# Kernel tuning notes

Measured on AMD Instinct MI355X. Metric: run time of the kernel, lower is better.

Reference implementation:

```python
import jax, jax.numpy as jnp
import numpy as np

N_NODES = 100000
N_EDGES = 3200000
F_IN = 256
H1 = 128   # growth_rate * bn_size
H2 = 32    # growth_rate
BN_EPS = 1e-5


def _gin_bn_relu(x, edge_index, Wa, ba, Wb, bb, gamma, beta):
    # GINConv (eps=0): h_i = MLP(x_i + sum_{j in N(i)} x_j)
    src, dst = edge_index[0], edge_index[1]
    agg = jax.ops.segment_sum(x[src], dst, num_segments=x.shape[0])  # [N, F]
    h = x + agg
    # nn1: Linear -> ReLU -> Linear
    h = jnp.maximum(h @ Wa + ba, 0.0)
    h = h @ Wb + bb
    # BatchNorm1d (training-mode batch stats over nodes)
    mean = h.mean(axis=0)
    var = h.var(axis=0)  # biased, matches torch BN normalization
    h = (h - mean) * jax.lax.rsqrt(var + BN_EPS) * gamma + beta
    return jnp.maximum(h, 0.0)


def setup_inputs() -> dict:
    key = jax.random.key(0)
    ks = jax.random.split(key, 12)
    x = jax.random.normal(ks[0], (N_NODES, F_IN), dtype=jnp.float32)
    edge_index = jax.random.randint(ks[1], (2, N_EDGES), 0, N_NODES, dtype=jnp.int64)

    def lin(k, fin, fout):
        s = 1.0 / np.sqrt(fin)
        return jax.random.uniform(k, (fin, fout), jnp.float32, -s, s)

    return {
        "x": x,
        "edge_index": edge_index,
        "W1a": lin(ks[2], F_IN, H1), "b1a": jnp.zeros((H1,), jnp.float32),
        "W1b": lin(ks[3], H1, H1),   "b1b": jnp.zeros((H1,), jnp.float32),
        "g1": jnp.ones((H1,), jnp.float32), "be1": jnp.zeros((H1,), jnp.float32),
        "W2a": lin(ks[4], H1, H2),   "b2a": jnp.zeros((H2,), jnp.float32),
        "W2b": lin(ks[5], H2, H2),   "b2b": jnp.zeros((H2,), jnp.float32),
        "g2": jnp.ones((H2,), jnp.float32), "be2": jnp.zeros((H2,), jnp.float32),
    }


def reference(x, edge_index, W1a, b1a, W1b, b1b, g1, be1,
              W2a, b2a, W2b, b2b, g2, be2):
    # data.x is a single tensor -> [x]; torch.cat([x], 1) == x (concat is a no-op)
    h = _gin_bn_relu(x, edge_index, W1a, b1a, W1b, b1b, g1, be1)   # [N, 128]
    h = _gin_bn_relu(h, edge_index, W2a, b2a, W2b, b2b, g2, be2)   # [N, 32]
    return h
```

## Files before the change

### kernel.cpp

```cpp
#include <hip/hip_runtime.h>

#define F_IN 256
#define H1 128
#define H2 32
#define BN_EPS 1e-5f
#define BSHIFT 8
#define BCAP 16384
#define CHUNK 4096
#define NSHARD 8

typedef short bf16x8 __attribute__((ext_vector_type(8)));
typedef float f32x4 __attribute__((ext_vector_type(4)));

__device__ __forceinline__ ushort f2bf(float f) {
    uint u = __float_as_uint(f);
    return (ushort)((u + 0x7FFFu + ((u >> 16) & 1u)) >> 16);
}
__device__ __forceinline__ float bf2f(ushort h) {
    return __uint_as_float((uint)h << 16);
}
__device__ __forceinline__ uint pack2(float a, float b) {
    return (uint)f2bf(a) | ((uint)f2bf(b) << 16);
}
__device__ __forceinline__ void unpack2(uint u, float& a, float& b) {
    a = __uint_as_float(u << 16);
    b = __uint_as_float(u & 0xFFFF0000u);
}
__device__ __forceinline__ int clampN(int v, int N) {
    return v < 0 ? 0 : (v >= N ? N - 1 : v);
}

__global__ __launch_bounds__(256) void super0_k(
    const float* __restrict__ W1a, const float* __restrict__ W1b,
    const float* __restrict__ W2a, const float* __restrict__ W2b,
    ushort* __restrict__ w1aT, ushort* __restrict__ w1bT,
    ushort* __restrict__ w2aT, ushort* __restrict__ w2bT,
    int* __restrict__ bucket_cursor, float* __restrict__ sums1,
    float* __restrict__ sums2) {
    const int tid = threadIdx.x;
    if (blockIdx.x == 212) {
        for (int i = tid; i < 512; i += 256) bucket_cursor[i] = 0;
        for (int i = tid; i < NSHARD * 2 * H1; i += 256) sums1[i] = 0.f;
        for (int i = tid; i < NSHARD * 2 * H2; i += 256) sums2[i] = 0.f;
        return;
    }
    int idx = blockIdx.x * 256 + tid;
    if (idx < 32768) {
        int k = idx >> 7, c = idx & 127;
        w1aT[c * 256 + k] = f2bf(W1a[idx]);
    } else if (idx < 49152) {
        int t = idx - 32768;
        int k = t >> 7, c = t & 127;
        w1bT[c * 128 + k] = f2bf(W1b[t]);
    } else if (idx < 53248) {
        int t = idx - 49152;
        int k = t >> 5, c = t & 31;
        w2aT[c * 128 + k] = f2bf(W2a[t]);
    } else if (idx < 54272) {
        int t = idx - 53248;
        int k = t >> 5, c = t & 31;
        w2bT[c * 32 + k] = f2bf(W2b[t]);
    }
}

__global__ __launch_bounds__(256) void binA_k(const int* __restrict__ eb,
                                              int E, int N, int NBUCK,
                                              int* __restrict__ bucket_cursor,
                                              uint* __restrict__ rec) {
    __shared__ int lcnt[512];
    __shared__ int lbase[512];
    __shared__ uint lrec[CHUNK];
    __shared__ ushort lbk[CHUNK];
    __shared__ ushort lrk[CHUNK];
    __shared__ int nzf;
    const int tid = threadIdx.x;
    const int cbase = blockIdx.x * CHUNK;
    const int cnum = min(CHUNK, E - cbase);
    if (cnum <= 0) return;
    if (tid == 0) nzf = 0;
    __syncthreads();
    {
        int i = tid * (CHUNK / 256);
        if (i < cnum && eb[2 * (cbase + i) + 1] != 0) atomicAdd(&nzf, 1);
    }
    for (int i = tid; i < NBUCK; i += 256) lcnt[i] = 0;
    __syncthreads();
    const int is64 = (nzf == 0);
    for (int i = tid; i < cnum; i += 256) {
        int e = cbase + i;
        int s = is64 ? eb[2 * e] : eb[e];
        int d = is64 ? eb[2 * (E + e)] : eb[E + e];
        s = clampN(s, N);
        d = clampN(d, N);
        int bk = d >> BSHIFT;
        int rk = atomicAdd(&lcnt[bk], 1);
        lrec[i] = (uint)s | ((uint)(d & 255) << 17);
        lbk[i] = (ushort)bk;
        lrk[i] = (ushort)rk;
    }
    __syncthreads();
    for (int i = tid; i < NBUCK; i += 256)
        if (lcnt[i]) lbase[i] = atomicAdd(&bucket_cursor[i], lcnt[i]);
    __syncthreads();
    for (int i = tid; i < cnum; i += 256) {
        int bk = lbk[i];
        int pos = lbase[bk] + lrk[i];
        if (pos < BCAP) rec[(size_t)bk * BCAP + pos] = lrec[i];
    }
}

__global__ __launch_bounds__(256) void gemm1_k(const float* __restrict__ Af,
                                               const ushort* __restrict__ WT,
                                               ushort* __restrict__ outb, int N) {
    constexpr int K = F_IN, NC = H1, NF = NC / 16;
    const int lane = threadIdx.x & 63;
    const int wave = threadIdx.x >> 6;
    const int row0 = blockIdx.x * 64 + wave * 16;
    const int col = lane & 15;
    const int k0 = (lane >> 4) * 8;
    int arow = row0 + col;
    if (arow >= N) arow = N - 1;

    f32x4 acc[NF];
#pragma unroll
    for (int f = 0; f < NF; ++f) acc[f] = (f32x4){0.f, 0.f, 0.f, 0.f};
#pragma unroll
    for (int kc = 0; kc < K; kc += 32) {
        const float* ap = &Af[(size_t)arow * K + kc + k0];
        float4 p = *(const float4*)ap;
        float4 q = *(const float4*)(ap + 4);
        bf16x8 af;
        af[0] = (short)f2bf(p.x); af[1] = (short)f2bf(p.y);
        af[2] = (short)f2bf(p.z); af[3] = (short)f2bf(p.w);
        af[4] = (short)f2bf(q.x); af[5] = (short)f2bf(q.y);
        af[6] = (short)f2bf(q.z); af[7] = (short)f2bf(q.w);
#pragma unroll
        for (int f = 0; f < NF; ++f) {
            bf16x8 bf = *(const bf16x8*)&WT[(size_t)(f * 16 + col) * K + kc + k0];
            acc[f] = __builtin_amdgcn_mfma_f32_16x16x32_bf16(af, bf, acc[f], 0, 0, 0);
        }
    }
    const int crow = row0 + (lane >> 4) * 4;
#pragma unroll
    for (int f = 0; f < NF; ++f) {
        const int c = f * 16 + col;
#pragma unroll
        for (int j = 0; j < 4; ++j) {
            int rr = crow + j;
            if (rr < N) outb[(size_t)rr * NC + c] = f2bf(acc[f][j]);
        }
    }
}

__global__ __launch_bounds__(256) void binB_k(const uint* __restrict__ rec,
                                              const int* __restrict__ bucket_cursor,
                                              int N, int NBUCK,
                                              int* __restrict__ row_start,
                                              int* __restrict__ esrc) {
    __shared__ int cntA[256];
    __shared__ int cntB[256];
    __shared__ int red[256];
    const int bk = blockIdx.x;
    const int tid = threadIdx.x;
    int part = 0;
    for (int i = tid; i < bk; i += 256) {
        int c = bucket_cursor[i];
        part += (c < BCAP) ? c : BCAP;
    }
    red[tid] = part;
    __syncthreads();
    for (int s = 128; s > 0; s >>= 1) {
        if (tid < s) red[tid] += red[tid + s];
        __syncthreads();
    }
    const int base = red[0];
    int cnt = bucket_cursor[bk];
    if (cnt > BCAP) cnt = BCAP;
    if (bk == NBUCK - 1 && tid == 0) row_start[N] = base + cnt;

    const uint* r = rec + (size_t)bk * BCAP;
    cntA[tid] = 0;
    __syncthreads();
    for (int i = tid; i < cnt; i += 256) atomicAdd(&cntA[r[i] >> 17], 1);
    __syncthreads();
    int* src = cntA;
    int* dst = cntB;
    for (int off = 1; off < 256; off <<= 1) {
        int v = src[tid] + (tid >= off ? src[tid - off] : 0);
        __syncthreads();
        dst[tid] = v;
        __syncthreads();
        int* t = src; src = dst; dst = t;
    }
    const int n0 = bk << BSHIFT;
    {
        int node = n0 + tid;
        if (node < N) row_start[node] = base + (tid ? src[tid - 1] : 0);
    }
    dst[tid] = 0;
    __syncthreads();
    for (int i = tid; i < cnt; i += 256) {
        uint rv = r[i];
        int dl = rv >> 17;
        int rank = atomicAdd(&dst[dl], 1);
        esrc[base + (dl ? src[dl - 1] : 0) + rank] = (int)(rv & 0x1FFFFu);
    }
}

template <int NC, bool BIAS, bool OUT_BF16, bool STATS, int NF>
__device__ __forceinline__ void gemm_epilogue(f32x4* acc, const float* bias,
                                              void* outv, int N, int row0,
                                              int lane, float* sums) {
    __shared__ float ssum[NC];
    __shared__ float ssq[NC];
    if (STATS) {
        if (threadIdx.x < NC) { ssum[threadIdx.x] = 0.f; ssq[threadIdx.x] = 0.f; }
        __syncthreads();
    }
    const int col0 = lane & 15;
    const int crow = row0 + (lane >> 4) * 4;
#pragma unroll
    for (int f = 0; f < NF; ++f) {
        const int c = f * 16 + col0;
        float bv = BIAS ? bias[c] : 0.f;
        float sv = 0.f, qv = 0.f;
#pragma unroll
        for (int j = 0; j < 4; ++j) {
            int rr = crow + j;
            if (rr < N) {
                float v = acc[f][j] + bv;
                if (OUT_BF16) ((ushort*)outv)[(size_t)rr * NC + c] = f2bf(v);
                else          ((float*)outv)[(size_t)rr * NC + c] = v;
                if (STATS) { sv += v; qv += v * v; }
            }
        }
        if (STATS) {
            sv += __shfl_xor(sv, 16); sv += __shfl_xor(sv, 32);
            qv += __shfl_xor(qv, 16); qv += __shfl_xor(qv, 32);
            if ((lane >> 4) == 0) {
                atomicAdd(&ssum[c], sv);
                atomicAdd(&ssq[c], qv);
            }
        }
    }
    if (STATS) {
        __syncthreads();
        if (threadIdx.x < NC) {
            float* sh = sums + (blockIdx.x & (NSHARD - 1)) * 2 * NC;
            atomicAdd(&sh[threadIdx.x], ssum[threadIdx.x]);
            atomicAdd(&sh[NC + threadIdx.x], ssq[threadIdx.x]);
        }
    }
}

template <int K, int NC, bool BIAS, bool OUT_BF16, bool STATS>
__global__ __launch_bounds__(256) void gemm_mfma_k(const ushort* __restrict__ A,
                                                   const ushort* __restrict__ WT,
                                                   const float* __restrict__ bias,
                                                   void* __restrict__ outv, int N,
                                                   float* __restrict__ sums) {
    constexpr int NF = NC / 16;
    const int lane = threadIdx.x & 63;
    const int wave = threadIdx.x >> 6;
    const int row0 = blockIdx.x * 64 + wave * 16;
    const int col = lane & 15;
    const int k0 = (lane >> 4) * 8;
    int arow = row0 + col;
    if (arow >= N) arow = N - 1;

    f32x4 acc[NF];
#pragma unroll
    for (int f = 0; f < NF; ++f) acc[f] = (f32x4){0.f, 0.f, 0.f, 0.f};
#pragma unroll
    for (int kc = 0; kc < K; kc += 32) {
        bf16x8 af = *(const bf16x8*)&A[(size_t)arow * K + kc + k0];
#pragma unroll
        for (int f = 0; f < NF; ++f) {
            bf16x8 bf = *(const bf16x8*)&WT[(size_t)(f * 16 + col) * K + kc + k0];
            acc[f] = __builtin_amdgcn_mfma_f32_16x16x32_bf16(af, bf, acc[f], 0, 0, 0);
        }
    }
    gemm_epilogue<NC, BIAS, OUT_BF16, STATS, NF>(acc, bias, outv, N, row0, lane, sums);
}

template <int K, int NC, bool OUT_BF16>
__global__ __launch_bounds__(256) void gemm_mfma_bnA_k(const ushort* __restrict__ U,
                                                       const ushort* __restrict__ WT,
                                                       const float* __restrict__ sums,
                                                       const float* __restrict__ g,
                                                       const float* __restrict__ be,
                                                       int Nbn,
                                                       void* __restrict__ outv, int N) {
    constexpr int NF = NC / 16;
    __shared__ __align__(16) float lsc[K];
    __shared__ __align__(16) float lsh[K];
    const int tid = threadIdx.x;
    if (tid < K) {
        float s = 0.f, q = 0.f;
#pragma unroll
        for (int sh = 0; sh < NSHARD; ++sh) {
            s += sums[sh * 2 * K + tid];
            q += sums[sh * 2 * K + K + tid];
        }
        float inv_n = 1.f / (float)Nbn;
        float mean = s * inv_n;
        float var = q * inv_n - mean * mean;
        float sc = g[tid] * rsqrtf(var + BN_EPS);
        lsc[tid] = sc;
        lsh[tid] = be[tid] - mean * sc;
    }
    __syncthreads();

    const int lane = tid & 63;
    const int wave = tid >> 6;
    const int row0 = blockIdx.x * 64 + wave * 16;
    const int col = lane & 15;
    const int k0 = (lane >> 4) * 8;
    int arow = row0 + col;
    if (arow >= N) arow = N - 1;

    f32x4 acc[NF];
#pragma unroll
    for (int f = 0; f < NF; ++f) acc[f] = (f32x4){0.f, 0.f, 0.f, 0.f};
#pragma unroll
    for (int kc = 0; kc < K; kc += 32) {
        bf16x8 raw = *(const bf16x8*)&U[(size_t)arow * K + kc + k0];
        float4 c0 = *(const float4*)&lsc[kc + k0];
        float4 c1 = *(const float4*)&lsc[kc + k0 + 4];
        float4 h0 = *(const float4*)&lsh[kc + k0];
        float4 h1 = *(const float4*)&lsh[kc + k0 + 4];
        bf16x8 af;
        af[0] = (short)f2bf(fmaxf(bf2f((ushort)raw[0]) * c0.x + h0.x, 0.f));
        af[1] = (short)f2bf(fmaxf(bf2f((ushort)raw[1]) * c0.y + h0.y, 0.f));
        af[2] = (short)f2bf(fmaxf(bf2f((ushort)raw[2]) * c0.z + h0.z, 0.f));
        af[3] = (short)f2bf(fmaxf(bf2f((ushort)raw[3]) * c0.w + h0.w, 0.f));
        af[4] = (short)f2bf(fmaxf(bf2f((ushort)raw[4]) * c1.x + h1.x, 0.f));
        af[5] = (short)f2bf(fmaxf(bf2f((ushort)raw[5]) * c1.y + h1.y, 0.f));
        af[6] = (short)f2bf(fmaxf(bf2f((ushort)raw[6]) * c1.z + h1.z, 0.f));
        af[7] = (short)f2bf(fmaxf(bf2f((ushort)raw[7]) * c1.w + h1.w, 0.f));
#pragma unroll
        for (int f = 0; f < NF; ++f) {
            bf16x8 bf = *(const bf16x8*)&WT[(size_t)(f * 16 + col) * K + kc + k0];
            acc[f] = __builtin_amdgcn_mfma_f32_16x16x32_bf16(af, bf, acc[f], 0, 0, 0);
        }
    }
    gemm_epilogue<NC, false, OUT_BF16, false, NF>(acc, nullptr, outv, N, row0, lane, nullptr);
}

__global__ void agg_f128b_k(const ushort* __restrict__ T, const int* __restrict__ row_start,
                            const int* __restrict__ esrc, const float* __restrict__ bias,
                            ushort* __restrict__ out, int N) {
    const int hw = (blockIdx.x << 3) | (threadIdx.x >> 5);
    const int lane = threadIdx.x & 31;
    if (hw >= N) return;
    const uint2* T2 = (const uint2*)T;
    uint2 sv = T2[(size_t)hw * 32 + lane];
    float a0, a1, a2, a3;
    unpack2(sv.x, a0, a1);
    unpack2(sv.y, a2, a3);
    int p = row_start[hw];
    const int pe = row_start[hw + 1];
    for (; p + 7 < pe; p += 8) {
        int s0 = esrc[p],     s1 = esrc[p + 1], s2 = esrc[p + 2], s3 = esrc[p + 3];
        int s4 = esrc[p + 4], s5 = esrc[p + 5], s6 = esrc[p + 6], s7 = esrc[p + 7];
        uint2 v0 = T2[(size_t)s0 * 32 + lane];
        uint2 v1 = T2[(size_t)s1 * 32 + lane];
        uint2 v2 = T2[(size_t)s2 * 32 + lane];
        uint2 v3 = T2[(size_t)s3 * 32 + lane];
        uint2 v4 = T2[(size_t)s4 * 32 + lane];
        uint2 v5 = T2[(size_t)s5 * 32 + lane];
        uint2 v6 = T2[(size_t)s6 * 32 + lane];
        uint2 v7 = T2[(size_t)s7 * 32 + lane];
        float x0, x1, x2, x3;
        unpack2(v0.x, x0, x1); unpack2(v0.y, x2, x3);
        a0 += x0; a1 += x1; a2 += x2; a3 += x3;
        unpack2(v1.x, x0, x1); unpack2(v1.y, x2, x3);
        a0 += x0; a1 += x1; a2 += x2; a3 += x3;
        unpack2(v2.x, x0, x1); unpack2(v2.y, x2, x3);
        a0 += x0; a1 += x1; a2 += x2; a3 += x3;
        unpack2(v3.x, x0, x1); unpack2(v3.y, x2, x3);
        a0 += x0; a1 += x1; a2 += x2; a3 += x3;
        unpack2(v4.x, x0, x1); unpack2(v4.y, x2, x3);
        a0 += x0; a1 += x1; a2 += x2; a3 += x3;
        unpack2(v5.x, x0, x1); unpack2(v5.y, x2, x3);
        a0 += x0; a1 += x1; a2 += x2; a3 += x3;
        unpack2(v6.x, x0, x1); unpack2(v6.y, x2, x3);
        a0 += x0; a1 += x1; a2 += x2; a3 += x3;
        unpack2(v7.x, x0, x1); unpack2(v7.y, x2, x3);
        a0 += x0; a1 += x1; a2 += x2; a3 += x3;
    }
    for (; p < pe; ++p) {
        uint2 v = T2[(size_t)esrc[p] * 32 + lane];
        float x0, x1, x2, x3;
        unpack2(v.x, x0, x1); unpack2(v.y, x2, x3);
        a0 += x0; a1 += x1; a2 += x2; a3 += x3;
    }
    const float4 b = ((const float4*)bias)[lane];
    a0 = fmaxf(a0 + b.x, 0.f);
    a1 = fmaxf(a1 + b.y, 0.f);
    a2 = fmaxf(a2 + b.z, 0.f);
    a3 = fmaxf(a3 + b.w, 0.f);
    ((uint2*)out)[(size_t)hw * 32 + lane] = make_uint2(pack2(a0, a1), pack2(a2, a3));
}

__global__ void agg_f32b_k(const ushort* __restrict__ T, const int* __restrict__ row_start,
                           const int* __restrict__ esrc, const float* __restrict__ bias,
                           ushort* __restrict__ out, int N) {
    const int wid = (blockIdx.x << 2) | (threadIdx.x >> 6);
    const int lane = threadIdx.x & 63;
    const int g = lane >> 3, l8 = lane & 7;
    if (wid >= N) return;
    const uint2* T2 = (const uint2*)T;
    float a0 = 0.f, a1 = 0.f, a2 = 0.f, a3 = 0.f;
    const int p0 = row_start[wid];
    const int pe = row_start[wid + 1];
    for (int p = p0 + g; p < pe; p += 8) {
        uint2 v = T2[(size_t)esrc[p] * 8 + l8];
        float x0, x1, x2, x3;
        unpack2(v.x, x0, x1); unpack2(v.y, x2, x3);
        a0 += x0; a1 += x1; a2 += x2; a3 += x3;
    }
#pragma unroll
    for (int off = 8; off < 64; off <<= 1) {
        a0 += __shfl_xor(a0, off);
        a1 += __shfl_xor(a1, off);
        a2 += __shfl_xor(a2, off);
        a3 += __shfl_xor(a3, off);
    }
    if (g == 0) {
        uint2 sv = T2[(size_t)wid * 8 + l8];
        float s0, s1, s2, s3;
        unpack2(sv.x, s0, s1); unpack2(sv.y, s2, s3);
        const float4 b = ((const float4*)bias)[l8];
        a0 = fmaxf(a0 + s0 + b.x, 0.f);
        a1 = fmaxf(a1 + s1 + b.y, 0.f);
        a2 = fmaxf(a2 + s2 + b.z, 0.f);
        a3 = fmaxf(a3 + s3 + b.w, 0.f);
        ((uint2*)out)[(size_t)wid * 8 + l8] = make_uint2(pack2(a0, a1), pack2(a2, a3));
    }
}

template <int F>
__global__ void bnapply_fin_k(const float* __restrict__ U, const float* __restrict__ sums,
                              const float* __restrict__ g, const float* __restrict__ be,
                              int Nbn, float* __restrict__ out, int total4) {
    __shared__ __align__(16) float lsc[F];
    __shared__ __align__(16) float lsh[F];
    const int tid = threadIdx.x;
    if (tid < F) {
        float s = 0.f, q = 0.f;
#pragma unroll
        for (int sh = 0; sh < NSHARD; ++sh) {
            s += sums[sh * 2 * F + tid];
            q += sums[sh * 2 * F + F + tid];
        }
        float inv_n = 1.f / (float)Nbn;
        float mean = s * inv_n;
        float var = q * inv_n - mean * mean;
        float sc = g[tid] * rsqrtf(var + BN_EPS);
        lsc[tid] = sc;
        lsh[tid] = be[tid] - mean * sc;
    }
    __syncthreads();
    const float4* U4 = (const float4*)U;
    float4* O4 = (float4*)out;
    const int stride = gridDim.x * blockDim.x;
    for (int i = blockIdx.x * blockDim.x + tid; i < total4; i += stride) {
        int c4 = (i % (F / 4)) * 4;
        float4 u = U4[i];
        float4 sc = *(const float4*)&lsc[c4];
        float4 sh = *(const float4*)&lsh[c4];
        float4 o;
        o.x = fmaxf(u.x * sc.x + sh.x, 0.f);
        o.y = fmaxf(u.y * sc.y + sh.y, 0.f);
        o.z = fmaxf(u.z * sc.z + sh.z, 0.f);
        o.w = fmaxf(u.w * sc.w + sh.w, 0.f);
        O4[i] = o;
    }
}

extern "C" void kernel_launch(void* const* d_in, const int* in_sizes, int n_in,
                              void* d_out, int out_size, void* d_ws, size_t ws_size,
                              hipStream_t stream) {
    const float* x   = (const float*)d_in[0];
    const int*   eb  = (const int*)d_in[1];
    const float* W1a = (const float*)d_in[2];
    const float* b1a = (const float*)d_in[3];
    const float* W1b = (const float*)d_in[4];
    const float* b1b = (const float*)d_in[5];
    const float* g1  = (const float*)d_in[6];
    const float* be1 = (const float*)d_in[7];
    const float* W2a = (const float*)d_in[8];
    const float* b2a = (const float*)d_in[9];
    const float* W2b = (const float*)d_in[10];
    const float* b2b = (const float*)d_in[11];
    const float* g2  = (const float*)d_in[12];
    const float* be2 = (const float*)d_in[13];
    float* out = (float*)d_out;

    const int N = in_sizes[0] / F_IN;
    const int E = in_sizes[1] / 2;
    const int NBUCK = (N + 255) >> BSHIFT;

    char* w = (char*)d_ws;
    size_t off = 0;
    auto alloc = [&](size_t bytes) -> void* {
        void* p = w + off;
        off = (off + bytes + 255) & ~(size_t)255;
        return p;
    };
    ushort* B0 = (ushort*)alloc((size_t)N * H1 * 2);
    ushort* B1 = (ushort*)alloc((size_t)N * H1 * 2);
    char*   B2 = (char*)alloc((size_t)N * H1 * 4);
    ushort* u1b = (ushort*)B2;
    float*  u2  = (float*)B2;

    int* row_start = (int*)alloc((size_t)(N + 1) * 4);
    int* esrc      = (int*)alloc((size_t)E * 4);
    uint* rec      = (uint*)alloc((size_t)NBUCK * BCAP * 4);
    int* bucket_cursor = (int*)alloc(512 * 4);
    ushort* w1aT = (ushort*)alloc(F_IN * H1 * 2);
    ushort* w1bT = (ushort*)alloc(H1 * H1 * 2);
    ushort* w2aT = (ushort*)alloc(H1 * H2 * 2);
    ushort* w2bT = (ushort*)alloc(H2 * H2 * 2);
    float* sums1 = (float*)alloc(NSHARD * 2 * H1 * 4);
    float* sums2 = (float*)alloc(NSHARD * 2 * H2 * 4);

    const int GB = (E + CHUNK - 1) / CHUNK;
    const int G1 = (N + 63) / 64;

    super0_k<<<213, 256, 0, stream>>>(W1a, W1b, W2a, W2b, w1aT, w1bT, w2aT, w2bT,
                                      bucket_cursor, sums1, sums2);
    binA_k<<<GB, 256, 0, stream>>>(eb, E, N, NBUCK, bucket_cursor, rec);
    gemm1_k<<<G1, 256, 0, stream>>>(x, w1aT, B1, N);
    binB_k<<<NBUCK, 256, 0, stream>>>(rec, bucket_cursor, N, NBUCK, row_start, esrc);
    agg_f128b_k<<<(N + 7) / 8, 256, 0, stream>>>(B1, row_start, esrc, b1a, B0, N);
    gemm_mfma_k<H1, H1, true, true, true><<<G1, 256, 0, stream>>>(B0, w1bT, b1b, u1b, N, sums1);
    gemm_mfma_bnA_k<H1, H2, true><<<G1, 256, 0, stream>>>(u1b, w2aT, sums1, g1, be1, N, B1, N);
    agg_f32b_k<<<(N + 3) / 4, 256, 0, stream>>>(B1, row_start, esrc, b2a, B0, N);
    gemm_mfma_k<H2, H2, true, false, true><<<G1, 256, 0, stream>>>(B0, w2bT, b2b, u2, N, sums2);
    bnapply_fin_k<H2><<<3125, 256, 0, stream>>>(u2, sums2, g2, be2, N, out, N * H2 / 4);
}
```

Before: 387.8 us.

## Merge binB and gemm1 into one launch; rework binA as two-pass count/scatter

binA now counts bucket sizes in a first pass, reserves global ranges, then re-reads the edges and scatters records directly, so the per-chunk shared-memory record staging goes away and the chunk size doubles. binB and the first GEMM become one kernel that assigns blocks by index range, removing a launch and letting the two independent jobs overlap. In exchange, binA reads the destination indices twice, and the write order inside a bucket now depends on atomic order. That is harmless because binB re-sorts within each bucket.

```diff
diff --git a/kernel.cpp b/kernel.cpp
--- a/kernel.cpp
+++ b/kernel.cpp
@@ -6,7 +6,7 @@
 #define BN_EPS 1e-5f
 #define BSHIFT 8
 #define BCAP 16384
-#define CHUNK 4096
+#define CHUNK 8192
 #define NSHARD 8
 
 typedef short bf16x8 __attribute__((ext_vector_type(8)));
@@ -69,9 +69,6 @@
                                               uint* __restrict__ rec) {
     __shared__ int lcnt[512];
     __shared__ int lbase[512];
-    __shared__ uint lrec[CHUNK];
-    __shared__ ushort lbk[CHUNK];
-    __shared__ ushort lrk[CHUNK];
     __shared__ int nzf;
     const int tid = threadIdx.x;
     const int cbase = blockIdx.x * CHUNK;
@@ -86,6 +83,19 @@
     for (int i = tid; i < NBUCK; i += 256) lcnt[i] = 0;
     __syncthreads();
     const int is64 = (nzf == 0);
+    for (int i = tid; i < cnum; i += 256) {
+        int e = cbase + i;
+        int d = is64 ? eb[2 * (E + e)] : eb[E + e];
+        d = clampN(d, N);
+        atomicAdd(&lcnt[d >> BSHIFT], 1);
+    }
+    __syncthreads();
+    for (int i = tid; i < NBUCK; i += 256) {
+        int c = lcnt[i];
+        lbase[i] = c ? atomicAdd(&bucket_cursor[i], c) : 0;
+        lcnt[i] = 0;
+    }
+    __syncthreads();
     for (int i = tid; i < cnum; i += 256) {
         int e = cbase + i;
         int s = is64 ? eb[2 * e] : eb[e];
@@ -93,29 +103,73 @@
         s = clampN(s, N);
         d = clampN(d, N);
         int bk = d >> BSHIFT;
-        int rk = atomicAdd(&lcnt[bk], 1);
-        lrec[i] = (uint)s | ((uint)(d & 255) << 17);
-        lbk[i] = (ushort)bk;
-        lrk[i] = (ushort)rk;
-    }
-    __syncthreads();
-    for (int i = tid; i < NBUCK; i += 256)
-        if (lcnt[i]) lbase[i] = atomicAdd(&bucket_cursor[i], lcnt[i]);
-    __syncthreads();
-    for (int i = tid; i < cnum; i += 256) {
-        int bk = lbk[i];
-        int pos = lbase[bk] + lrk[i];
-        if (pos < BCAP) rec[(size_t)bk * BCAP + pos] = lrec[i];
-    }
-}
-
-__global__ __launch_bounds__(256) void gemm1_k(const float* __restrict__ Af,
-                                               const ushort* __restrict__ WT,
-                                               ushort* __restrict__ outb, int N) {
+        int pos = lbase[bk] + atomicAdd(&lcnt[bk], 1);
+        if (pos < BCAP)
+            rec[(size_t)bk * BCAP + pos] = (uint)s | ((uint)(d & 255) << 17);
+    }
+}
+
+__device__ __forceinline__ void binB_body(int bk, const uint* __restrict__ rec,
+                                          const int* __restrict__ bucket_cursor,
+                                          int N, int NBUCK,
+                                          int* __restrict__ row_start,
+                                          int* __restrict__ esrc) {
+    __shared__ int cntA[256];
+    __shared__ int cntB[256];
+    __shared__ int red[256];
+    const int tid = threadIdx.x;
+    int part = 0;
+    for (int i = tid; i < bk; i += 256) {
+        int c = bucket_cursor[i];
+        part += (c < BCAP) ? c : BCAP;
+    }
+    red[tid] = part;
+    __syncthreads();
+    for (int s = 128; s > 0; s >>= 1) {
+        if (tid < s) red[tid] += red[tid + s];
+        __syncthreads();
+    }
+    const int base = red[0];
+    int cnt = bucket_cursor[bk];
+    if (cnt > BCAP) cnt = BCAP;
+    if (bk == NBUCK - 1 && tid == 0) row_start[N] = base + cnt;
+
+    const uint* r = rec + (size_t)bk * BCAP;
+    cntA[tid] = 0;
+    __syncthreads();
+    for (int i = tid; i < cnt; i += 256) atomicAdd(&cntA[r[i] >> 17], 1);
+    __syncthreads();
+    int* src = cntA;
+    int* dst = cntB;
+    for (int off = 1; off < 256; off <<= 1) {
+        int v = src[tid] + (tid >= off ? src[tid - off] : 0);
+        __syncthreads();
+        dst[tid] = v;
+        __syncthreads();
+        int* t = src; src = dst; dst = t;
+    }
+    const int n0 = bk << BSHIFT;
+    {
+        int node = n0 + tid;
+        if (node < N) row_start[node] = base + (tid ? src[tid - 1] : 0);
+    }
+    dst[tid] = 0;
+    __syncthreads();
+    for (int i = tid; i < cnt; i += 256) {
+        uint rv = r[i];
+        int dl = rv >> 17;
+        int rank = atomicAdd(&dst[dl], 1);
+        esrc[base + (dl ? src[dl - 1] : 0) + rank] = (int)(rv & 0x1FFFFu);
+    }
+}
+
+__device__ __forceinline__ void gemm1_body(int bid, const float* __restrict__ Af,
+                                           const ushort* __restrict__ WT,
+                                           ushort* __restrict__ outb, int N) {
     constexpr int K = F_IN, NC = H1, NF = NC / 16;
     const int lane = threadIdx.x & 63;
     const int wave = threadIdx.x >> 6;
-    const int row0 = blockIdx.x * 64 + wave * 16;
+    const int row0 = bid * 64 + wave * 16;
     const int col = lane & 15;
     const int k0 = (lane >> 4) * 8;
     int arow = row0 + col;
@@ -152,59 +206,15 @@
     }
 }
 
-__global__ __launch_bounds__(256) void binB_k(const uint* __restrict__ rec,
-                                              const int* __restrict__ bucket_cursor,
-                                              int N, int NBUCK,
-                                              int* __restrict__ row_start,
-                                              int* __restrict__ esrc) {
-    __shared__ int cntA[256];
-    __shared__ int cntB[256];
-    __shared__ int red[256];
-    const int bk = blockIdx.x;
-    const int tid = threadIdx.x;
-    int part = 0;
-    for (int i = tid; i < bk; i += 256) {
-        int c = bucket_cursor[i];
-        part += (c < BCAP) ? c : BCAP;
-    }
-    red[tid] = part;
-    __syncthreads();
-    for (int s = 128; s > 0; s >>= 1) {
-        if (tid < s) red[tid] += red[tid + s];
-        __syncthreads();
-    }
-    const int base = red[0];
-    int cnt = bucket_cursor[bk];
-    if (cnt > BCAP) cnt = BCAP;
-    if (bk == NBUCK - 1 && tid == 0) row_start[N] = base + cnt;
-
-    const uint* r = rec + (size_t)bk * BCAP;
-    cntA[tid] = 0;
-    __syncthreads();
-    for (int i = tid; i < cnt; i += 256) atomicAdd(&cntA[r[i] >> 17], 1);
-    __syncthreads();
-    int* src = cntA;
-    int* dst = cntB;
-    for (int off = 1; off < 256; off <<= 1) {
-        int v = src[tid] + (tid >= off ? src[tid - off] : 0);
-        __syncthreads();
-        dst[tid] = v;
-        __syncthreads();
-        int* t = src; src = dst; dst = t;
-    }
-    const int n0 = bk << BSHIFT;
-    {
-        int node = n0 + tid;
-        if (node < N) row_start[node] = base + (tid ? src[tid - 1] : 0);
-    }
-    dst[tid] = 0;
-    __syncthreads();
-    for (int i = tid; i < cnt; i += 256) {
-        uint rv = r[i];
-        int dl = rv >> 17;
-        int rank = atomicAdd(&dst[dl], 1);
-        esrc[base + (dl ? src[dl - 1] : 0) + rank] = (int)(rv & 0x1FFFFu);
-    }
+__global__ __launch_bounds__(256) void super2_k(
+    const uint* __restrict__ rec, const int* __restrict__ bucket_cursor,
+    int N, int NBUCK, int* __restrict__ row_start, int* __restrict__ esrc,
+    const float* __restrict__ x, const ushort* __restrict__ w1aT,
+    ushort* __restrict__ t1b) {
+    if ((int)blockIdx.x < NBUCK)
+        binB_body(blockIdx.x, rec, bucket_cursor, N, NBUCK, row_start, esrc);
+    else
+        gemm1_body(blockIdx.x - NBUCK, x, w1aT, t1b, N);
 }
 
 template <int NC, bool BIAS, bool OUT_BF16, bool STATS, int NF>
@@ -532,8 +542,8 @@
     super0_k<<<213, 256, 0, stream>>>(W1a, W1b, W2a, W2b, w1aT, w1bT, w2aT, w2bT,
                                       bucket_cursor, sums1, sums2);
     binA_k<<<GB, 256, 0, stream>>>(eb, E, N, NBUCK, bucket_cursor, rec);
-    gemm1_k<<<G1, 256, 0, stream>>>(x, w1aT, B1, N);
-    binB_k<<<NBUCK, 256, 0, stream>>>(rec, bucket_cursor, N, NBUCK, row_start, esrc);
+    super2_k<<<NBUCK + G1, 256, 0, stream>>>(rec, bucket_cursor, N, NBUCK,
+                                             row_start, esrc, x, w1aT, B1);
     agg_f128b_k<<<(N + 7) / 8, 256, 0, stream>>>(B1, row_start, esrc, b1a, B0, N);
     gemm_mfma_k<H1, H1, true, true, true><<<G1, 256, 0, stream>>>(B0, w1bT, b1b, u1b, N, sums1);
     gemm_mfma_bnA_k<H1, H2, true><<<G1, 256, 0, stream>>>(u1b, w2aT, sums1, g1, be1, N, B1, N);
```

Measured after the change: 395.5 us. No clear change (+2.0%).

## Fuse CSR bucket finalize with first GEMM and sub-sort edges by source octant

Applied to the files above, without the earlier changes.

Merges the bucket-finalize (binB) and first dense GEMM into one launch, splitting blocks by index so CSR construction and the x@W1a MFMA GEMM run concurrently and one launch gap disappears. binB now sorts each destination's edges into 8 sub-bins by source-index high bits, so neighbour gathers within a row touch nearby source rows. The row-start array grows to 8 entries per node and the aggregation kernels read the stride-8 layout. The cost is larger LDS use in the fused kernel, which can lower occupancy for the GEMM blocks, and a bigger row-start buffer.

```diff
diff --git a/kernel.cpp b/kernel.cpp
--- a/kernel.cpp
+++ b/kernel.cpp
@@ -109,13 +109,80 @@
     }
 }
 
-__global__ __launch_bounds__(256) void gemm1_k(const float* __restrict__ Af,
-                                               const ushort* __restrict__ WT,
-                                               ushort* __restrict__ outb, int N) {
+__device__ __forceinline__ void binB_body(int bk, const uint* __restrict__ rec,
+                                          const int* __restrict__ bucket_cursor,
+                                          int N, int NBUCK,
+                                          int* __restrict__ rs2,
+                                          int* __restrict__ esrc) {
+    __shared__ int cnt[2048];
+    __shared__ int rnk[2048];
+    __shared__ int red[256];
+    const int tid = threadIdx.x;
+    int part = 0;
+    for (int i = tid; i < bk; i += 256) {
+        int c = bucket_cursor[i];
+        part += (c < BCAP) ? c : BCAP;
+    }
+    red[tid] = part;
+    __syncthreads();
+    for (int s = 128; s > 0; s >>= 1) {
+        if (tid < s) red[tid] += red[tid + s];
+        __syncthreads();
+    }
+    const int base = red[0];
+    __syncthreads();
+    int cntb = bucket_cursor[bk];
+    if (cntb > BCAP) cntb = BCAP;
+    if (bk == NBUCK - 1 && tid == 0) rs2[(size_t)N * 8] = base + cntb;
+
+    const uint* r = rec + (size_t)bk * BCAP;
+    for (int i = tid; i < 2048; i += 256) { cnt[i] = 0; rnk[i] = 0; }
+    __syncthreads();
+    for (int i = tid; i < cntb; i += 256) {
+        uint rv = r[i];
+        atomicAdd(&cnt[((rv >> 17) << 3) | ((rv >> 14) & 7u)], 1);
+    }
+    __syncthreads();
+    int loc[8];
+    int s = 0;
+#pragma unroll
+    for (int j = 0; j < 8; ++j) { loc[j] = s; s += cnt[tid * 8 + j]; }
+    const int tot = s;
+    red[tid] = tot;
+    __syncthreads();
+    for (int off = 1; off < 256; off <<= 1) {
+        int t = (tid >= off) ? red[tid - off] : 0;
+        __syncthreads();
+        red[tid] += t;
+        __syncthreads();
+    }
+    const int excl_t = red[tid] - tot;
+    __syncthreads();
+    const int n0 = bk << BSHIFT;
+#pragma unroll
+    for (int j = 0; j < 8; ++j) {
+        int b = tid * 8 + j;
+        int ex = excl_t + loc[j];
+        cnt[b] = ex;
+        int node = n0 + (b >> 3);
+        if (node < N) rs2[(size_t)node * 8 + (b & 7)] = base + ex;
+    }
+    __syncthreads();
+    for (int i = tid; i < cntb; i += 256) {
+        uint rv = r[i];
+        int b = ((rv >> 17) << 3) | ((rv >> 14) & 7u);
+        int pos = cnt[b] + atomicAdd(&rnk[b], 1);
+        esrc[base + pos] = (int)(rv & 0x1FFFFu);
+    }
+}
+
+__device__ __forceinline__ void gemm1_body(int bid, const float* __restrict__ Af,
+                                           const ushort* __restrict__ WT,
+                                           ushort* __restrict__ outb, int N) {
     constexpr int K = F_IN, NC = H1, NF = NC / 16;
     const int lane = threadIdx.x & 63;
     const int wave = threadIdx.x >> 6;
-    const int row0 = blockIdx.x * 64 + wave * 16;
+    const int row0 = bid * 64 + wave * 16;
     const int col = lane & 15;
     const int k0 = (lane >> 4) * 8;
     int arow = row0 + col;
@@ -152,59 +219,15 @@
     }
 }
 
-__global__ __launch_bounds__(256) void binB_k(const uint* __restrict__ rec,
-                                              const int* __restrict__ bucket_cursor,
-                                              int N, int NBUCK,
-                                              int* __restrict__ row_start,
-                                              int* __restrict__ esrc) {
-    __shared__ int cntA[256];
-    __shared__ int cntB[256];
-    __shared__ int red[256];
-    const int bk = blockIdx.x;
-    const int tid = threadIdx.x;
-    int part = 0;
-    for (int i = tid; i < bk; i += 256) {
-        int c = bucket_cursor[i];
-        part += (c < BCAP) ? c : BCAP;
-    }
-    red[tid] = part;
-    __syncthreads();
-    for (int s = 128; s > 0; s >>= 1) {
-        if (tid < s) red[tid] += red[tid + s];
-        __syncthreads();
-    }
-    const int base = red[0];
-    int cnt = bucket_cursor[bk];
-    if (cnt > BCAP) cnt = BCAP;
-    if (bk == NBUCK - 1 && tid == 0) row_start[N] = base + cnt;
-
-    const uint* r = rec + (size_t)bk * BCAP;
-    cntA[tid] = 0;
-    __syncthreads();
-    for (int i = tid; i < cnt; i += 256) atomicAdd(&cntA[r[i] >> 17], 1);
-    __syncthreads();
-    int* src = cntA;
-    int* dst = cntB;
-    for (int off = 1; off < 256; off <<= 1) {
-        int v = src[tid] + (tid >= off ? src[tid - off] : 0);
-        __syncthreads();
-        dst[tid] = v;
-        __syncthreads();
-        int* t = src; src = dst; dst = t;
-    }
-    const int n0 = bk << BSHIFT;
-    {
-        int node = n0 + tid;
-        if (node < N) row_start[node] = base + (tid ? src[tid - 1] : 0);
-    }
-    dst[tid] = 0;
-    __syncthreads();
-    for (int i = tid; i < cnt; i += 256) {
-        uint rv = r[i];
-        int dl = rv >> 17;
-        int rank = atomicAdd(&dst[dl], 1);
-        esrc[base + (dl ? src[dl - 1] : 0) + rank] = (int)(rv & 0x1FFFFu);
-    }
+__global__ __launch_bounds__(256) void super2_k(
+    const uint* __restrict__ rec, const int* __restrict__ bucket_cursor,
+    int N, int NBUCK, int* __restrict__ rs2, int* __restrict__ esrc,
+    const float* __restrict__ x, const ushort* __restrict__ w1aT,
+    ushort* __restrict__ t1b) {
+    if ((int)blockIdx.x < NBUCK)
+        binB_body(blockIdx.x, rec, bucket_cursor, N, NBUCK, rs2, esrc);
+    else
+        gemm1_body(blockIdx.x - NBUCK, x, w1aT, t1b, N);
 }
 
 template <int NC, bool BIAS, bool OUT_BF16, bool STATS, int NF>
@@ -347,7 +370,7 @@
     gemm_epilogue<NC, false, OUT_BF16, false, NF>(acc, nullptr, outv, N, row0, lane, nullptr);
 }
 
-__global__ void agg_f128b_k(const ushort* __restrict__ T, const int* __restrict__ row_start,
+__global__ void agg_f128b_k(const ushort* __restrict__ T, const int* __restrict__ rs2,
                             const int* __restrict__ esrc, const float* __restrict__ bias,
                             ushort* __restrict__ out, int N) {
     const int hw = (blockIdx.x << 3) | (threadIdx.x >> 5);
@@ -358,8 +381,8 @@
     float a0, a1, a2, a3;
     unpack2(sv.x, a0, a1);
     unpack2(sv.y, a2, a3);
-    int p = row_start[hw];
-    const int pe = row_start[hw + 1];
+    int p = rs2[(size_t)hw * 8];
+    const int pe = rs2[(size_t)hw * 8 + 8];
     for (; p + 7 < pe; p += 8) {
         int s0 = esrc[p],     s1 = esrc[p + 1], s2 = esrc[p + 2], s3 = esrc[p + 3];
         int s4 = esrc[p + 4], s5 = esrc[p + 5], s6 = esrc[p + 6], s7 = esrc[p + 7];
@@ -403,7 +426,7 @@
     ((uint2*)out)[(size_t)hw * 32 + lane] = make_uint2(pack2(a0, a1), pack2(a2, a3));
 }
 
-__global__ void agg_f32b_k(const ushort* __restrict__ T, const int* __restrict__ row_start,
+__global__ void agg_f32b_k(const ushort* __restrict__ T, const int* __restrict__ rs2,
                            const int* __restrict__ esrc, const float* __restrict__ bias,
                            ushort* __restrict__ out, int N) {
     const int wid = (blockIdx.x << 2) | (threadIdx.x >> 6);
@@ -412,8 +435,8 @@
     if (wid >= N) return;
     const uint2* T2 = (const uint2*)T;
     float a0 = 0.f, a1 = 0.f, a2 = 0.f, a3 = 0.f;
-    const int p0 = row_start[wid];
-    const int pe = row_start[wid + 1];
+    const int p0 = rs2[(size_t)wid * 8];
+    const int pe = rs2[(size_t)wid * 8 + 8];
     for (int p = p0 + g; p < pe; p += 8) {
         uint2 v = T2[(size_t)esrc[p] * 8 + l8];
         float x0, x1, x2, x3;
@@ -515,7 +538,7 @@
     ushort* u1b = (ushort*)B2;
     float*  u2  = (float*)B2;
 
-    int* row_start = (int*)alloc((size_t)(N + 1) * 4);
+    int* rs2       = (int*)alloc(((size_t)N * 8 + 1) * 4);
     int* esrc      = (int*)alloc((size_t)E * 4);
     uint* rec      = (uint*)alloc((size_t)NBUCK * BCAP * 4);
     int* bucket_cursor = (int*)alloc(512 * 4);
@@ -532,12 +555,12 @@
     super0_k<<<213, 256, 0, stream>>>(W1a, W1b, W2a, W2b, w1aT, w1bT, w2aT, w2bT,
                                       bucket_cursor, sums1, sums2);
     binA_k<<<GB, 256, 0, stream>>>(eb, E, N, NBUCK, bucket_cursor, rec);
-    gemm1_k<<<G1, 256, 0, stream>>>(x, w1aT, B1, N);
-    binB_k<<<NBUCK, 256, 0, stream>>>(rec, bucket_cursor, N, NBUCK, row_start, esrc);
-    agg_f128b_k<<<(N + 7) / 8, 256, 0, stream>>>(B1, row_start, esrc, b1a, B0, N);
+    super2_k<<<NBUCK + G1, 256, 0, stream>>>(rec, bucket_cursor, N, NBUCK,
+                                             rs2, esrc, x, w1aT, B1);
+    agg_f128b_k<<<(N + 7) / 8, 256, 0, stream>>>(B1, rs2, esrc, b1a, B0, N);
     gemm_mfma_k<H1, H1, true, true, true><<<G1, 256, 0, stream>>>(B0, w1bT, b1b, u1b, N, sums1);
     gemm_mfma_bnA_k<H1, H2, true><<<G1, 256, 0, stream>>>(u1b, w2aT, sums1, g1, be1, N, B1, N);
-    agg_f32b_k<<<(N + 3) / 4, 256, 0, stream>>>(B1, row_start, esrc, b2a, B0, N);
+    agg_f32b_k<<<(N + 3) / 4, 256, 0, stream>>>(B1, rs2, esrc, b2a, B0, N);
     gemm_mfma_k<H2, H2, true, false, true><<<G1, 256, 0, stream>>>(B0, w2bT, b2b, u2, N, sums2);
     bnapply_fin_k<H2><<<3125, 256, 0, stream>>>(u2, sums2, g2, be2, N, out, N * H2 / 4);
 }
```

After: 370.2 us (median of 2 runs). 1.05x faster.
